# Kernel optimization log

Measured on AMD Instinct MI355X. Metric: run time of the kernel, lower is better.

The kernel has to match this reference:

```python
import jax, jax.numpy as jnp
import numpy as np

NUM_NODES = 4096
N_REL = 5          # in_channels: number of relation adjacencies in A
N_CH = 2           # out_channels: number of meta-path channels
N_EDGES = 131072   # edges per relation (avg degree 32)
THRESHOLD = 0.05   # GTLayer threshold


def _dense_adj(edge_index, edge_value, num_nodes):
    # Coalesce (op='add') each relation's edge list into a dense [N,N] adjacency.
    # edge_index: [R, 2, E] int, edge_value: [R, E] float -> [R, N, N]
    def one(ei, ev):
        return jnp.zeros((num_nodes, num_nodes), ev.dtype).at[ei[0], ei[1]].add(ev)
    return jax.vmap(one)(edge_index, edge_value)


def setup_inputs() -> dict:
    key = jax.random.key(0)
    k1, k2, k3, k4 = jax.random.split(key, 4)
    edge_index = jax.random.randint(k1, (N_REL, 2, N_EDGES), 0, NUM_NODES)
    edge_value = jax.random.uniform(k2, (N_REL, N_EDGES), dtype=jnp.float32)
    # GTConv weights: nn.init.normal_(std=0.01), shape [out_channels, in_channels]
    w1 = jax.random.normal(k3, (N_CH, N_REL), dtype=jnp.float32) * 0.01
    w2 = jax.random.normal(k4, (N_CH, N_REL), dtype=jnp.float32) * 0.01
    return {"edge_index": edge_index, "edge_value": edge_value,
            "w1": w1, "w2": w2, "num_nodes": NUM_NODES}


def reference(edge_index, edge_value, w1, w2, num_nodes):
    # GTLayer(first=True).forward(A, num_nodes)
    A = _dense_adj(edge_index, edge_value, num_nodes)       # [R, N, N]
    F1 = jax.nn.softmax(w1, axis=1)                          # [C, R]
    F2 = jax.nn.softmax(w2, axis=1)                          # [C, R]
    # GTConv: softmax-weighted sum of relation adjacencies (concat+coalesce add)
    A1 = jnp.einsum('cr,rmn->cmn', F1, A)                    # [C, N, N]
    A2 = jnp.einsum('cr,rmn->cmn', F2, A)                    # [C, N, N]
    # spspmm per channel, then threshold: keep values > threshold
    H = jnp.einsum('cmk,ckn->cmn', A1, A2)                   # [C, N, N]
    H = jnp.where(H > THRESHOLD, H, jnp.zeros((), H.dtype))
    # keep_rate == 1 -> top-k pruning branch is a no-op (skipped, as in source)
    return (H, F1, F2)
```

## Files before the change

### kernel.cpp

```cpp
#include <hip/hip_runtime.h>
#include <math.h>

#define N 4096
#define NREL 5
#define NCH 2
#define NEDGE 131072
#define THRESH 0.05f
#define FSCALE 268435456.0f
#define INV_FSCALE_F (1.0f/268435456.0f)
#define INV_P56 (1.0/72057594037927936.0)
#define ROWCAP 192
#define KCAP   320

#define THRQ    13421773
#define MARGINQ 128
#define OVERQ   536870912u
#define WLCAP   2048

#define CNT_OFF  ((size_t)0)
#define WLC_OFF  ((size_t)(2 * N))
#define WL_OFF   ((size_t)(2 * N + 1))
#define P8_OFF   ((size_t)16384)
#define NENT     ((size_t)N * 2 * ROWCAP)
#define E2_OFF   (P8_OFF + NENT * 2)
#define Q1B_OFF  (E2_OFF + NENT * 4)
#define F_OFF    (Q1B_OFF + NENT)

__global__ void softmax_kernel(const float* __restrict__ w1,
                               const float* __restrict__ w2,
                               float* __restrict__ F,
                               float* __restrict__ out_tail) {
    int c = threadIdx.x;
    if (c < 2 * NCH) {
        const float* w = (c < NCH) ? w1 : w2;
        int row = c % NCH;
        int base = (c < NCH) ? 0 : NCH * NREL;
        float m = -1e30f;
        for (int r = 0; r < NREL; ++r) m = fmaxf(m, w[row * NREL + r]);
        float e[NREL];
        float s = 0.f;
        for (int r = 0; r < NREL; ++r) { e[r] = expf(w[row * NREL + r] - m); s += e[r]; }
        float inv = 1.0f / s;
        for (int r = 0; r < NREL; ++r) {
            float f = e[r] * inv;
            F[base + row * NREL + r] = f;
            out_tail[base + row * NREL + r] = f;
        }
    }
}

__global__ void scatter_csr(const int* __restrict__ ei,
                            const float* __restrict__ ev,
                            const float* __restrict__ F,
                            int* __restrict__ CNT,
                            unsigned long long* __restrict__ P8,
                            int4* __restrict__ E2,
                            int* __restrict__ Q1B) {
    int t = blockIdx.x * blockDim.x + threadIdx.x;
    if (t >= NREL * NEDGE) return;
    int r = t / NEDGE;
    int e = t - r * NEDGE;
    int i = ei[(size_t)(r * 2 + 0) * NEDGE + e];
    int j = ei[(size_t)(r * 2 + 1) * NEDGE + e];
    float v = ev[(size_t)r * NEDGE + e];
    int h  = j >> 11;
    int jl = j & 2047;
    int pos = atomicAdd(&CNT[i * 2 + h], 1);
    if (pos < ROWCAP) {
        size_t idx = ((size_t)i * 2 + h) * ROWCAP + pos;
        int q1a = __float2int_rn(F[0 * NREL + r] * v * FSCALE);
        int q1b = __float2int_rn(F[1 * NREL + r] * v * FSCALE);
        int q2a = __float2int_rn(F[NCH * NREL + 0 * NREL + r] * v * FSCALE);
        int q2b = __float2int_rn(F[NCH * NREL + 1 * NREL + r] * v * FSCALE);
        unsigned q2ap = ((unsigned)q2a + 4u) >> 3;
        unsigned q2bp = ((unsigned)q2b + 4u) >> 3;
        P8[idx] = (unsigned long long)jl
                | ((unsigned long long)q2ap << 11)
                | ((unsigned long long)q2bp << 37);
        E2[idx]  = make_int4(jl, q2a, q2b, q1a);
        Q1B[idx] = q1b;
    }
}

__launch_bounds__(256, 8)
__global__ void spgemm_approx(const int* __restrict__ CNT,
                              const unsigned long long* __restrict__ P8,
                              const int4* __restrict__ E2,
                              const int* __restrict__ Q1B,
                              float* __restrict__ out,
                              int* __restrict__ WLC,
                              int* __restrict__ WL) {
    __shared__ unsigned long long acc[2048];
    __shared__ int2 kA[KCAP];
    __shared__ unsigned short kK[KCAP];
    __shared__ unsigned char  kCt[KCAP];
    __shared__ int blkflag;
    const int m = blockIdx.x;
    const int h = blockIdx.y;

    for (int i = threadIdx.x; i < 2048; i += 256) acc[i] = 0ULL;
    if (threadIdx.x == 0) blkflag = 0;

    int nk0 = min(CNT[m * 2 + 0], ROWCAP);
    int nk1 = min(CNT[m * 2 + 1], ROWCAP);
    int nk = min(nk0 + nk1, KCAP);
    for (int i = threadIdx.x; i < nk; i += 256) {
        int b  = (i >= nk0) ? 1 : 0;
        int ii = i - (b ? nk0 : 0);
        size_t idx = ((size_t)m * 2 + b) * ROWCAP + ii;
        int4 e4 = E2[idx];
        int k = e4.x + (b << 11);
        kK[i]  = (unsigned short)k;
        kCt[i] = (unsigned char)min(CNT[k * 2 + h], ROWCAP);
        kA[i]  = make_int2(e4.w, Q1B[idx]);
    }
    __syncthreads();

    const int slot = threadIdx.x >> 5;
    const int lane = threadIdx.x & 31;

#define PROC(eu, ax, ay)                                                        \
    {                                                                           \
        unsigned col = (unsigned)(eu) & 2047u;                                  \
        unsigned qa  = (unsigned)((eu) >> 11) & 0x3FFFFFFu;                     \
        unsigned qb  = (unsigned)((eu) >> 37);                                  \
        unsigned ua = (unsigned)(((unsigned long long)(unsigned)(ax) * qa       \
                                  + (1ULL << 24)) >> 25);                       \
        unsigned ub = (unsigned)(((unsigned long long)(unsigned)(ay) * qb       \
                                  + (1ULL << 24)) >> 25);                       \
        atomicAdd(&acc[col],                                                    \
                  (unsigned long long)ua | ((unsigned long long)ub << 32));     \
    }

    for (int ki = slot; ki < nk; ki += 16) {
        int cntA = kCt[ki];
        int2 aA = kA[ki];
        const ulonglong2* __restrict__ rowA =
            (const ulonglong2*)(P8 + ((size_t)kK[ki] * 2 + h) * ROWCAP);

        int kiB = ki + 8;
        bool hasB = kiB < nk;
        int cntB = hasB ? kCt[kiB] : 0;
        int2 aB = hasB ? kA[kiB] : make_int2(0, 0);
        const ulonglong2* __restrict__ rowB =
            (const ulonglong2*)(P8 + ((size_t)(hasB ? kK[kiB] : 0) * 2 + h) * ROWCAP);

        int PA = (cntA + 1) >> 1;
        int PB = (cntB + 1) >> 1;
        int P  = (PA > PB) ? PA : PB;
        for (int p = lane; p < P; p += 32) {
            ulonglong2 ea, eb;
            bool vA = p < PA, vB = p < PB;
            if (vA) ea = rowA[p];
            if (vB) eb = rowB[p];
            if (vA) {
                PROC(ea.x, aA.x, aA.y);
                if (2 * p + 1 < cntA) PROC(ea.y, aA.x, aA.y);
            }
            if (vB) {
                PROC(eb.x, aB.x, aB.y);
                if (2 * p + 1 < cntB) PROC(eb.y, aB.x, aB.y);
            }
        }
    }
#undef PROC
    __syncthreads();

    float* orow0 = out + (size_t)0 * N * N + (size_t)m * N + ((size_t)h << 11);
    float* orow1 = out + (size_t)1 * N * N + (size_t)m * N + ((size_t)h << 11);
    bool f0 = false, f1 = false;
    for (int t = threadIdx.x; t < 512; t += 256) {
        float4 h0, h1;
        float* p0 = (float*)&h0;
        float* p1 = (float*)&h1;
#pragma unroll
        for (int u = 0; u < 4; ++u) {
            unsigned long long v = acc[t * 4 + u];
            unsigned lo = (unsigned)v;
            unsigned hi = (unsigned)(v >> 32);
            int d0 = (int)lo - THRQ;
            int d1 = (int)hi - THRQ;
            f0 |= (d0 <= MARGINQ && d0 >= -MARGINQ) || (lo >= OVERQ);
            f1 |= (d1 <= MARGINQ && d1 >= -MARGINQ) || (hi >= OVERQ);
            float x0 = (float)lo * INV_FSCALE_F;
            float x1 = (float)hi * INV_FSCALE_F;
            p0[u] = (x0 > THRESH) ? x0 : 0.f;
            p1[u] = (x1 > THRESH) ? x1 : 0.f;
        }
        *(float4*)&orow0[t * 4] = h0;
        *(float4*)&orow1[t * 4] = h1;
    }
    if (f0) atomicOr(&blkflag, 1);
    if (f1) atomicOr(&blkflag, 2);
    __syncthreads();
    if (threadIdx.x == 0 && blkflag) {
        if (blkflag & 1) {
            int pos = atomicAdd(WLC, 1);
            if (pos < WLCAP) WL[pos] = (m << 2) | (h << 1) | 0;
        }
        if (blkflag & 2) {
            int pos = atomicAdd(WLC, 1);
            if (pos < WLCAP) WL[pos] = (m << 2) | (h << 1) | 1;
        }
    }
}

__launch_bounds__(256, 8)
__global__ void spgemm_exact(const int* __restrict__ CNT,
                             const int4* __restrict__ E2,
                             const int* __restrict__ Q1B,
                             float* __restrict__ out,
                             const int* __restrict__ WLC,
                             const int* __restrict__ WL) {
    int nwl = min(*WLC, WLCAP);
    if ((int)blockIdx.x >= nwl) return;
    int wl = WL[blockIdx.x];
    int m = wl >> 2;
    int h = (wl >> 1) & 1;
    int c = wl & 1;

    __shared__ unsigned long long acc[2048];
    __shared__ int kAc[KCAP];
    __shared__ unsigned short kK[KCAP];
    __shared__ unsigned char  kCt[KCAP];

    for (int i = threadIdx.x; i < 2048; i += 256) acc[i] = 0ULL;

    int nk0 = min(CNT[m * 2 + 0], ROWCAP);
    int nk1 = min(CNT[m * 2 + 1], ROWCAP);
    int nk = min(nk0 + nk1, KCAP);
    for (int i = threadIdx.x; i < nk; i += 256) {
        int b  = (i >= nk0) ? 1 : 0;
        int ii = i - (b ? nk0 : 0);
        size_t idx = ((size_t)m * 2 + b) * ROWCAP + ii;
        int4 e4 = E2[idx];
        int k = e4.x + (b << 11);
        kK[i]  = (unsigned short)k;
        kCt[i] = (unsigned char)min(CNT[k * 2 + h], ROWCAP);
        kAc[i] = c ? Q1B[idx] : e4.w;
    }
    __syncthreads();

    const int slot = threadIdx.x >> 5;
    const int lane = threadIdx.x & 31;
    const char* __restrict__ base = (const char*)E2;

    for (int ki = slot; ki < nk; ki += 16) {
        int cntA = kCt[ki];
        long long aA = (long long)kAc[ki];
        const int4* __restrict__ rowA = (const int4*)
            (base + (unsigned)(((int)kK[ki] * 2 + h) * (ROWCAP * 16)));

        int kiB = ki + 8;
        bool hasB = kiB < nk;
        int cntB = hasB ? kCt[kiB] : 0;
        long long aB = hasB ? (long long)kAc[kiB] : 0;
        const int4* __restrict__ rowB = (const int4*)
            (base + (unsigned)((((int)(hasB ? kK[kiB] : 0)) * 2 + h) * (ROWCAP * 16)));

        int P = (cntA > cntB) ? cntA : cntB;
        for (int p = lane; p < P; p += 32) {
            int4 qa, qb;
            bool vA = p < cntA, vB = p < cntB;
            if (vA) qa = rowA[p];
            if (vB) qb = rowB[p];
            if (vA) {
                int q2 = c ? qa.z : qa.y;
                atomicAdd(&acc[qa.x], (unsigned long long)(aA * (long long)q2));
            }
            if (vB) {
                int q2 = c ? qb.z : qb.y;
                atomicAdd(&acc[qb.x], (unsigned long long)(aB * (long long)q2));
            }
        }
    }
    __syncthreads();

    float* orow = out + (size_t)c * N * N + (size_t)m * N + ((size_t)h << 11);
    for (int t = threadIdx.x; t < 512; t += 256) {
        float4 hv;
        float* hp = (float*)&hv;
#pragma unroll
        for (int u = 0; u < 4; ++u) {
            double d = (double)(long long)acc[t * 4 + u] * INV_P56;
            float f = (float)d;
            hp[u] = (f > THRESH) ? f : 0.f;
        }
        *(float4*)&orow[t * 4] = hv;
    }
}

extern "C" void kernel_launch(void* const* d_in, const int* in_sizes, int n_in,
                              void* d_out, int out_size, void* d_ws, size_t ws_size,
                              hipStream_t stream) {
    const int*   ei = (const int*)d_in[0];
    const float* ev = (const float*)d_in[1];
    const float* w1 = (const float*)d_in[2];
    const float* w2 = (const float*)d_in[3];
    float* out = (float*)d_out;

    int*   wsI = (int*)d_ws;
    int*   CNT = wsI + CNT_OFF;
    int*   WLC = wsI + WLC_OFF;
    int*   WL  = wsI + WL_OFF;
    unsigned long long* P8 = (unsigned long long*)(wsI + P8_OFF);
    int4*  E2  = (int4*)(wsI + E2_OFF);
    int*   Q1B = wsI + Q1B_OFF;
    float* F   = (float*)(wsI + F_OFF);

    float* out_tail = out + (size_t)NCH * N * N;
    softmax_kernel<<<1, 64, 0, stream>>>(w1, w2, F, out_tail);

    hipMemsetAsync(wsI, 0, (size_t)(2 * N + 1) * sizeof(int), stream);

    int total_edges = NREL * NEDGE;
    scatter_csr<<<(total_edges + 255) / 256, 256, 0, stream>>>(ei, ev, F, CNT, P8, E2, Q1B);

    spgemm_approx<<<dim3(N, 2), 256, 0, stream>>>(CNT, P8, E2, Q1B, out, WLC, WL);
    spgemm_exact<<<WLCAP, 256, 0, stream>>>(CNT, E2, Q1B, out, WLC, WL);
}
```

Baseline: 171.1 us.

## Repack P8 with 21-bit weights and remap SpGEMM to 16-lane row groups

The packed B-entry format now stores the two channel weights at 21-bit precision in aligned 32-bit halves, so decoding needs fewer shifts and masks. The product rounding shift and the recheck margin are widened to match. The inner SpGEMM loop drops the paired-row scheme (one 32-lane slot handling rows ki and ki+8) and instead gives each k-row to a 16-lane group, which cuts predication and lane waste on short rows. This trades weight precision for cheaper decode and may send more entries to the exact recheck path.

```diff
diff --git a/kernel.cpp b/kernel.cpp
--- a/kernel.cpp
+++ b/kernel.cpp
@@ -13,7 +13,7 @@
 #define KCAP   320
 
 #define THRQ    13421773
-#define MARGINQ 128
+#define MARGINQ 256
 #define OVERQ   536870912u
 #define WLCAP   2048
 
@@ -72,11 +72,10 @@
         int q1b = __float2int_rn(F[1 * NREL + r] * v * FSCALE);
         int q2a = __float2int_rn(F[NCH * NREL + 0 * NREL + r] * v * FSCALE);
         int q2b = __float2int_rn(F[NCH * NREL + 1 * NREL + r] * v * FSCALE);
-        unsigned q2ap = ((unsigned)q2a + 4u) >> 3;
-        unsigned q2bp = ((unsigned)q2b + 4u) >> 3;
-        P8[idx] = (unsigned long long)jl
-                | ((unsigned long long)q2ap << 11)
-                | ((unsigned long long)q2bp << 37);
+        unsigned qa21 = ((unsigned)q2a + 16u) >> 5;
+        unsigned qb21 = ((unsigned)q2b + 16u) >> 5;
+        unsigned w0 = (unsigned)jl | (qa21 << 11);
+        P8[idx] = (unsigned long long)w0 | ((unsigned long long)qb21 << 32);
         E2[idx]  = make_int4(jl, q2a, q2b, q1a);
         Q1B[idx] = q1b;
     }
@@ -116,20 +115,23 @@
     }
     __syncthreads();
 
-    const int slot = threadIdx.x >> 5;
-    const int lane = threadIdx.x & 31;
-
-#define PROC(eu, ax, ay)                                                        \
+    const int slot = threadIdx.x >> 4;
+    const int lane = threadIdx.x & 15;
+
+#define PROC(eu, a0, a1)                                                        \
     {                                                                           \
-        unsigned col = (unsigned)(eu) & 2047u;                                  \
-        unsigned qa  = (unsigned)((eu) >> 11) & 0x3FFFFFFu;                     \
-        unsigned qb  = (unsigned)((eu) >> 37);                                  \
-        unsigned ua = (unsigned)(((unsigned long long)(unsigned)(ax) * qa       \
-                                  + (1ULL << 24)) >> 25);                       \
-        unsigned ub = (unsigned)(((unsigned long long)(unsigned)(ay) * qb       \
-                                  + (1ULL << 24)) >> 25);                       \
+        unsigned w0  = (unsigned)(eu);                                          \
+        unsigned w1  = (unsigned)((eu) >> 32);                                  \
+        unsigned col = w0 & 2047u;                                              \
+        unsigned qa  = w0 >> 11;                                                \
+        unsigned long long pA =                                                 \
+            (unsigned long long)(unsigned)(a0) * qa + (1u << 22);               \
+        unsigned long long pB =                                                 \
+            (unsigned long long)(unsigned)(a1) * w1 + (1u << 22);               \
+        unsigned uA = (unsigned)(pA >> 23);                                     \
+        unsigned uB = (unsigned)(pB >> 23);                                     \
         atomicAdd(&acc[col],                                                    \
-                  (unsigned long long)ua | ((unsigned long long)ub << 32));     \
+                  (unsigned long long)uA | ((unsigned long long)uB << 32));     \
     }
 
     for (int ki = slot; ki < nk; ki += 16) {
@@ -137,30 +139,11 @@
         int2 aA = kA[ki];
         const ulonglong2* __restrict__ rowA =
             (const ulonglong2*)(P8 + ((size_t)kK[ki] * 2 + h) * ROWCAP);
-
-        int kiB = ki + 8;
-        bool hasB = kiB < nk;
-        int cntB = hasB ? kCt[kiB] : 0;
-        int2 aB = hasB ? kA[kiB] : make_int2(0, 0);
-        const ulonglong2* __restrict__ rowB =
-            (const ulonglong2*)(P8 + ((size_t)(hasB ? kK[kiB] : 0) * 2 + h) * ROWCAP);
-
         int PA = (cntA + 1) >> 1;
-        int PB = (cntB + 1) >> 1;
-        int P  = (PA > PB) ? PA : PB;
-        for (int p = lane; p < P; p += 32) {
-            ulonglong2 ea, eb;
-            bool vA = p < PA, vB = p < PB;
-            if (vA) ea = rowA[p];
-            if (vB) eb = rowB[p];
-            if (vA) {
-                PROC(ea.x, aA.x, aA.y);
-                if (2 * p + 1 < cntA) PROC(ea.y, aA.x, aA.y);
-            }
-            if (vB) {
-                PROC(eb.x, aB.x, aB.y);
-                if (2 * p + 1 < cntB) PROC(eb.y, aB.x, aB.y);
-            }
+        for (int p = lane; p < PA; p += 16) {
+            ulonglong2 e = rowA[p];
+            PROC(e.x, aA.x, aA.y);
+            if (2 * p + 1 < cntA) PROC(e.y, aA.x, aA.y);
         }
     }
 #undef PROC
```

After: 162.2 us. -5.2%, faster.
